# Kernel optimization log

Measured on AMD Instinct MI355X. Metric: run time of the kernel, lower is better.

Reference implementation:

```python
import jax, jax.numpy as jnp
import numpy as np

ND = 3       # ndims
Q = 8        # mixture components
LAT = 64     # latent_dim
N = 2048     # num X points
M = 2048     # num Y points
TRI = ND * (ND + 1) // 2  # 6

_TI, _TJ = np.tril_indices(ND)


def setup_inputs() -> dict:
    key = jax.random.key(0)
    ks = jax.random.split(key, 10)
    s_in = 1.0 / np.sqrt(ND)
    s_lat = 1.0 / np.sqrt(LAT)
    return {
        "x": jax.random.normal(ks[0], (N, ND), jnp.float32),
        "y": jax.random.normal(ks[1], (M, ND), jnp.float32),
        "W1": jax.random.normal(ks[2], (LAT, ND), jnp.float32) * s_in,
        "b1": jax.random.normal(ks[3], (LAT,), jnp.float32) * 0.1,
        "Ww": jax.random.normal(ks[4], (Q, LAT), jnp.float32) * s_lat,
        "bw": jax.random.normal(ks[5], (Q,), jnp.float32) * 0.1,
        "Wf": jax.random.normal(ks[6], (Q * ND, LAT), jnp.float32) * s_lat,
        "bf": jax.random.normal(ks[7], (Q * ND,), jnp.float32) * 0.1,
        "Ws": jax.random.normal(ks[8], (Q * TRI, LAT), jnp.float32) * s_lat,
        "bs": jax.random.normal(ks[9], (Q * TRI,), jnp.float32) * 0.1,
    }


def _features(p, W1, b1, Ww, bw, Wf, bf, Ws, bs):
    # shared hidden layer (computed once per point, unlike the original which
    # recomputes it for each of the 3 heads -- same math)
    h = jax.nn.selu(p @ W1.T + b1)                                  # [n, LAT]
    w = jax.nn.softplus(h @ Ww.T + bw)                              # [n, Q]
    f = jax.nn.softplus(h @ Wf.T + bf).reshape(p.shape[0], Q, ND)   # [n, Q, ND]
    s = jax.nn.softplus(h @ Ws.T + bs).reshape(p.shape[0], Q, TRI)  # [n, Q, TRI]
    # place into lower-triangular L, then A = L @ L.T
    L = jnp.zeros((p.shape[0], Q, ND, ND), p.dtype).at[:, :, _TI, _TJ].set(s)
    A = jnp.einsum('nqab,nqcb->nqac', L, L)                         # [n, Q, ND, ND]
    phase = jnp.einsum('nqd,nd->nq', f, p)                          # [n, Q]
    return w, A, phase


def reference(x, y, W1, b1, Ww, bw, Wf, bf, Ws, bs):
    # __call__ -> k_xy[i, j] = eval(x=Y[j], y=X[i]); shape [N, M]
    wX, AX, phX = _features(x, W1, b1, Ww, bw, Wf, bf, Ws, bs)
    wY, AY, phY = _features(y, W1, b1, Ww, bw, Wf, bf, Ws, bs)

    diff = y[None, :, :] - x[:, None, :]                            # [N, M, ND]
    # r_scaled = diff @ (A_x + A_y) @ diff, split into the two quadratic forms
    qx = jnp.einsum('ijd,iqde,ije->ijq', diff, AX, diff)            # [N, M, Q]
    qy = jnp.einsum('ijd,jqde,ije->ijq', diff, AY, diff)            # [N, M, Q]
    r = qx + qy

    sq5 = jnp.sqrt(jnp.asarray(5.0, r.dtype))
    mat = (1.0 + sq5 * r + (5.0 / 3.0) * r * r) * jnp.exp(-sq5 * r)
    cosine = jnp.cos(2.0 * jnp.pi * (phY[None, :, :] - phX[:, None, :]))
    k = jnp.sum(wY[None, :, :] * wX[:, None, :] * mat * cosine, axis=-1)
    return k
```

## Files before the change

### kernel.cpp

```cpp
#include <hip/hip_runtime.h>
#include <hip/hip_bf16.h>

#define NPTS 2048
#define QMIX 8
#define LATD 64
#define IT   32
#define HIT  16
#define FSTRIDE 72

typedef float v2f __attribute__((ext_vector_type(2)));

__device__ __forceinline__ float softplus_f(float x) {
    return fmaxf(x, 0.0f) + log1pf(expf(-fabsf(x)));
}
__device__ __forceinline__ float selu_f(float z) {
    const float sc = 1.0507009873554805f;
    const float sa = 1.7580993408473766f;
    return (z > 0.0f) ? sc * z : sa * expm1f(z);
}

__global__ __launch_bounds__(640) void feat_kernel(
    const float* __restrict__ xin, const float* __restrict__ yin,
    const float* __restrict__ W1, const float* __restrict__ b1,
    const float* __restrict__ Ww, const float* __restrict__ bw,
    const float* __restrict__ Wf, const float* __restrict__ bf,
    const float* __restrict__ Ws, const float* __restrict__ bs,
    float* __restrict__ F)
{
    __shared__ float hsh[8][LATD + 4];
    __shared__ float raw[8][80];
    const int t = threadIdx.x;

    if (t < 512) {
        const int pl = t & 7, l = t >> 3;
        const int g = blockIdx.x * 8 + pl;
        const bool isx = (g < NPTS);
        const float* pts = isx ? (xin + 3 * g) : (yin + 3 * (g - NPTS));
        const float z = fmaf(W1[l * 3 + 0], pts[0],
                        fmaf(W1[l * 3 + 1], pts[1],
                        fmaf(W1[l * 3 + 2], pts[2], b1[l])));
        hsh[pl][l] = selu_f(z);
    }
    __syncthreads();

    {
        const int o  = t >> 3;
        const int pl = t & 7;
        const int q  = o / 10;
        const int e  = o % 10;
        const float* row;
        float acc;
        if (e == 0)      { row = Ww + q * LATD;                 acc = bw[q]; }
        else if (e <= 3) { row = Wf + (q * 3 + (e - 1)) * LATD; acc = bf[q * 3 + (e - 1)]; }
        else             { row = Ws + (q * 6 + (e - 4)) * LATD; acc = bs[q * 6 + (e - 4)]; }
#pragma unroll
        for (int l4 = 0; l4 < LATD / 4; ++l4) {
            const float4 rv = reinterpret_cast<const float4*>(row)[l4];
            const float4 hv = *reinterpret_cast<const float4*>(&hsh[pl][l4 * 4]);
            acc = fmaf(rv.x, hv.x, acc);
            acc = fmaf(rv.y, hv.y, acc);
            acc = fmaf(rv.z, hv.z, acc);
            acc = fmaf(rv.w, hv.w, acc);
        }
        raw[pl][o] = softplus_f(acc);
    }
    __syncthreads();

    if (t < 64) {
        const int pl2 = t >> 3, q2 = t & 7;
        const int g2  = blockIdx.x * 8 + pl2;
        const bool isx2 = (g2 < NPTS);
        const float* pts2 = isx2 ? (xin + 3 * g2) : (yin + 3 * (g2 - NPTS));
        const float c0 = pts2[0], c1 = pts2[1], c2 = pts2[2];
        const float* r = raw[pl2] + q2 * 10;
        const float w  = r[0];
        const float f0 = r[1], f1 = r[2], f2 = r[3];
        const float s0 = r[4], s1 = r[5], s2 = r[6];
        const float s3 = r[7], s4 = r[8], s5 = r[9];

        const float A00 = s0 * s0;
        const float A11 = fmaf(s1, s1, s2 * s2);
        const float A22 = fmaf(s3, s3, fmaf(s4, s4, s5 * s5));
        const float A01 = s0 * s1;
        const float A02 = s0 * s3;
        const float A12 = fmaf(s1, s3, s2 * s4);
        const float ph  = fmaf(f0, c0, fmaf(f1, c1, f2 * c2));
        float sn, cs;
        sincosf(6.283185307179586477f * ph, &sn, &cs);

        const float EF  = 3.2259751249059600974f;
        const float EF2 = 2.0f * EF;
        const float vals[8] = { EF * A00, EF * A11, EF * A22,
                                EF2 * A01, EF2 * A02, EF2 * A12,
                                w * cs, w * sn };
        float* o = F + (size_t)g2 * FSTRIDE;
        const int base = (q2 >> 1) * 16 + (q2 & 1);
#pragma unroll
        for (int k = 0; k < 8; ++k) o[base + k * 2] = vals[k];
        if (q2 == 0) {
            o[64] = c0; o[65] = c0;
            o[66] = c1; o[67] = c1;
            o[68] = c2; o[69] = c2;
        }
    }
}

__global__ __launch_bounds__(256, 4) void pair_kernel(
    const float* __restrict__ F, float* __restrict__ out)
{
    __shared__ float red[HIT][128];
    const int t    = threadIdx.x;
    const int wave = __builtin_amdgcn_readfirstlane(t >> 6);
    const int lane = t & 63;
    const int qg   = wave & 1;
    const int jh   = wave >> 1;
    const int jl   = jh * 64 + lane;
    const int j    = blockIdx.x * 128 + jl;
    const int i0   = blockIdx.y * IT;

    const float* __restrict__ frow = F + (size_t)(NPTS + j) * FSTRIDE;
    v2f fy[16];
    {
        const float4* fp = reinterpret_cast<const float4*>(frow + qg * 32);
#pragma unroll
        for (int n = 0; n < 8; ++n) {
            const float4 v = fp[n];
            fy[2 * n + 0] = v2f{v.x, v.y};
            fy[2 * n + 1] = v2f{v.z, v.w};
        }
    }
    const v2f yd0 = *reinterpret_cast<const v2f*>(frow + 64);
    const v2f yd1 = *reinterpret_cast<const v2f*>(frow + 66);
    const v2f yd2 = *reinterpret_cast<const v2f*>(frow + 68);

    const float P1 = 0.69314718055994530942f;
    const float P2 = 0.16013630893549922444f;
    const float* __restrict__ fxb = F + (size_t)i0 * FSTRIDE;

#pragma unroll
    for (int half = 0; half < 2; ++half) {
        v2f acc[HIT];
#pragma unroll
        for (int i2 = 0; i2 < HIT; ++i2) {
            const float* __restrict__ fx = fxb + (half * HIT + i2) * FSTRIDE;
            const v2f xd0 = *reinterpret_cast<const v2f*>(fx + 64);
            const v2f xd1 = *reinterpret_cast<const v2f*>(fx + 66);
            const v2f xd2 = *reinterpret_cast<const v2f*>(fx + 68);
            const v2f d0 = yd0 - xd0;
            const v2f d1 = yd1 - xd1;
            const v2f d2 = yd2 - xd2;
            const v2f p00 = d0 * d0, p11 = d1 * d1, p22 = d2 * d2;
            const v2f p01 = d0 * d1, p02 = d0 * d2, p12 = d1 * d2;

            v2f a = v2f{0.f, 0.f};
#pragma unroll
            for (int qpl = 0; qpl < 2; ++qpl) {
                const v2f* __restrict__ c =
                    reinterpret_cast<const v2f*>(fx + (qg * 2 + qpl) * 16);
                v2f u;
                u  = (fy[qpl * 8 + 0] + c[0]) * p00;
                u += (fy[qpl * 8 + 1] + c[1]) * p11;
                u += (fy[qpl * 8 + 2] + c[2]) * p22;
                u += (fy[qpl * 8 + 3] + c[3]) * p01;
                u += (fy[qpl * 8 + 4] + c[4]) * p02;
                u += (fy[qpl * 8 + 5] + c[5]) * p12;
                const v2f poly = u * (u * P2 + P1) + 1.0f;
                const v2f ex = v2f{__builtin_amdgcn_exp2f(-u.x),
                                   __builtin_amdgcn_exp2f(-u.y)};
                v2f ct = fy[qpl * 8 + 6] * c[6];
                ct += fy[qpl * 8 + 7] * c[7];
                a += (poly * ex) * ct;
            }
            acc[i2] = a;
        }

        if (qg == 1) {
#pragma unroll
            for (int i2 = 0; i2 < HIT; ++i2)
                red[i2][jl] = acc[i2].x + acc[i2].y;
        }
        __syncthreads();
        if (qg == 0) {
#pragma unroll
            for (int i2 = 0; i2 < HIT; ++i2) {
                out[(size_t)(i0 + half * HIT + i2) * NPTS + j] =
                    acc[i2].x + acc[i2].y + red[i2][jl];
            }
        }
        __syncthreads();
    }
}

extern "C" void kernel_launch(void* const* d_in, const int* in_sizes, int n_in,
                              void* d_out, int out_size, void* d_ws, size_t ws_size,
                              hipStream_t stream) {
    const float* x  = (const float*)d_in[0];
    const float* y  = (const float*)d_in[1];
    const float* W1 = (const float*)d_in[2];
    const float* b1 = (const float*)d_in[3];
    const float* Ww = (const float*)d_in[4];
    const float* bw = (const float*)d_in[5];
    const float* Wf = (const float*)d_in[6];
    const float* bf = (const float*)d_in[7];
    const float* Ws = (const float*)d_in[8];
    const float* bs = (const float*)d_in[9];
    float* out = (float*)d_out;

    float* F = (float*)d_ws;

    feat_kernel<<<dim3((2 * NPTS) / 8), dim3(640), 0, stream>>>(
        x, y, W1, b1, Ww, bw, Wf, bf, Ws, bs, F);

    pair_kernel<<<dim3(NPTS / 128, NPTS / IT), dim3(256), 0, stream>>>(F, out);
}
```

Baseline: 34.24 us.

## Recast pairwise quadratic forms as bf16x3 MFMA matrix products

The quadratic form (y-x)^T(Ax+Ay)(y-x) is expanded algebraically into a 10-term dot product between per-point coefficient and monomial vectors. Those vectors are split into hi/lo bf16 pairs so the pair kernel can compute the quadratic forms with 16x16x32 bf16 MFMA instructions. The cosine weight term becomes a small MFMA built from packed cos/sin weights. X tiles are staged in swizzled LDS. This moves the pairwise arithmetic onto matrix cores. In exchange it adds precision risk from the bf16 splitting, from cancellation in the expanded form, and from rounding the weights to bf16, and the new layout enlarges the workspace.

```diff
diff --git a/kernel.cpp b/kernel.cpp
--- a/kernel.cpp
+++ b/kernel.cpp
@@ -4,11 +4,10 @@
 #define NPTS 2048
 #define QMIX 8
 #define LATD 64
-#define IT   32
-#define HIT  16
-#define FSTRIDE 72
-
-typedef float v2f __attribute__((ext_vector_type(2)));
+#define NIT  4
+
+typedef float f32x4 __attribute__((ext_vector_type(4)));
+typedef short short8 __attribute__((ext_vector_type(8)));
 
 __device__ __forceinline__ float softplus_f(float x) {
     return fmaxf(x, 0.0f) + log1pf(expf(-fabsf(x)));
@@ -17,6 +16,16 @@
     const float sc = 1.0507009873554805f;
     const float sa = 1.7580993408473766f;
     return (z > 0.0f) ? sc * z : sa * expm1f(z);
+}
+__device__ __forceinline__ ushort bfrn(float v) {
+    unsigned b = __float_as_uint(v);
+    return (ushort)((b + 0x7fffu + ((b >> 16) & 1u)) >> 16);
+}
+__device__ __forceinline__ void split_bf16(float v, ushort& h, ushort& l) {
+    unsigned b  = __float_as_uint(v);
+    unsigned hb = b & 0xffff0000u;
+    h = (ushort)(hb >> 16);
+    l = bfrn(v - __uint_as_float(hb));
 }
 
 __global__ __launch_bounds__(640) void feat_kernel(
@@ -25,7 +34,9 @@
     const float* __restrict__ Ww, const float* __restrict__ bw,
     const float* __restrict__ Wf, const float* __restrict__ bf,
     const float* __restrict__ Ws, const float* __restrict__ bs,
-    float* __restrict__ F)
+    ushort* __restrict__ AXH, ushort* __restrict__ AXL,
+    ushort* __restrict__ BYH, ushort* __restrict__ BYL,
+    uint* __restrict__ CTX, uint* __restrict__ CTY)
 {
     __shared__ float hsh[8][LATD + 4];
     __shared__ float raw[8][80];
@@ -72,122 +83,133 @@
         const bool isx2 = (g2 < NPTS);
         const float* pts2 = isx2 ? (xin + 3 * g2) : (yin + 3 * (g2 - NPTS));
         const float c0 = pts2[0], c1 = pts2[1], c2 = pts2[2];
-        const float* r = raw[pl2] + q2 * 10;
-        const float w  = r[0];
-        const float f0 = r[1], f1 = r[2], f2 = r[3];
-        const float s0 = r[4], s1 = r[5], s2 = r[6];
-        const float s3 = r[7], s4 = r[8], s5 = r[9];
+        const float* rr = raw[pl2] + q2 * 10;
+        const float w  = rr[0];
+        const float f0 = rr[1], f1 = rr[2], f2 = rr[3];
+        const float s0 = rr[4], s1 = rr[5], s2 = rr[6];
+        const float s3 = rr[7], s4 = rr[8], s5 = rr[9];
 
         const float A00 = s0 * s0;
-        const float A11 = fmaf(s1, s1, s2 * s2);
-        const float A22 = fmaf(s3, s3, fmaf(s4, s4, s5 * s5));
         const float A01 = s0 * s1;
         const float A02 = s0 * s3;
+        const float A11 = fmaf(s1, s1, s2 * s2);
         const float A12 = fmaf(s1, s3, s2 * s4);
+        const float A22 = fmaf(s3, s3, fmaf(s4, s4, s5 * s5));
+        const float Ax0 = fmaf(A00, c0, fmaf(A01, c1, A02 * c2));
+        const float Ax1 = fmaf(A01, c0, fmaf(A11, c1, A12 * c2));
+        const float Ax2 = fmaf(A02, c0, fmaf(A12, c1, A22 * c2));
+        const float pAp = fmaf(c0, Ax0, fmaf(c1, Ax1, c2 * Ax2));
         const float ph  = fmaf(f0, c0, fmaf(f1, c1, f2 * c2));
         float sn, cs;
         sincosf(6.283185307179586477f * ph, &sn, &cs);
 
-        const float EF  = 3.2259751249059600974f;
-        const float EF2 = 2.0f * EF;
-        const float vals[8] = { EF * A00, EF * A11, EF * A22,
-                                EF2 * A01, EF2 * A02, EF2 * A12,
-                                w * cs, w * sn };
-        float* o = F + (size_t)g2 * FSTRIDE;
-        const int base = (q2 >> 1) * 16 + (q2 & 1);
-#pragma unroll
-        for (int k = 0; k < 8; ++k) o[base + k * 2] = vals[k];
-        if (q2 == 0) {
-            o[64] = c0; o[65] = c0;
-            o[66] = c1; o[67] = c1;
-            o[68] = c2; o[69] = c2;
-        }
+        const float EF = 3.2259751249059600974f;
+        const float cf[10] = { EF * A00, EF * A11, EF * A22,
+                               2.0f * EF * A01, 2.0f * EF * A02, 2.0f * EF * A12,
+                               -2.0f * EF * Ax0, -2.0f * EF * Ax1, -2.0f * EF * Ax2,
+                               EF * pAp };
+        const float pv[10] = { c0 * c0, c1 * c1, c2 * c2,
+                               c0 * c1, c0 * c2, c1 * c2,
+                               c0, c1, c2, 1.0f };
+        float slots[20];
+#pragma unroll
+        for (int k = 0; k < 10; ++k) {
+            slots[k]      = isx2 ? cf[k] : pv[k];
+            slots[10 + k] = isx2 ? pv[k] : cf[k];
+        }
+        ushort H[32], L[32];
+#pragma unroll
+        for (int k = 0; k < 32; ++k) { H[k] = 0; L[k] = 0; }
+#pragma unroll
+        for (int k = 0; k < 20; ++k) split_bf16(slots[k], H[k], L[k]);
+
+        const int pi = isx2 ? g2 : (g2 - NPTS);
+        ushort* dh = (isx2 ? AXH : BYH) + ((size_t)pi * 8 + q2) * 32;
+        ushort* dl = (isx2 ? AXL : BYL) + ((size_t)pi * 8 + q2) * 32;
+#pragma unroll
+        for (int m = 0; m < 16; ++m) {
+            ((uint*)dh)[m] = (uint)H[2 * m] | ((uint)H[2 * m + 1] << 16);
+            ((uint*)dl)[m] = (uint)L[2 * m] | ((uint)L[2 * m + 1] << 16);
+        }
+        uint* ct = isx2 ? CTX : CTY;
+        ct[(size_t)pi * 8 + q2] = (uint)bfrn(w * cs) | ((uint)bfrn(w * sn) << 16);
     }
 }
 
 __global__ __launch_bounds__(256, 4) void pair_kernel(
-    const float* __restrict__ F, float* __restrict__ out)
+    const ushort* __restrict__ AXH, const ushort* __restrict__ AXL,
+    const uint*  __restrict__ CTX,
+    const ushort* __restrict__ BYH, const ushort* __restrict__ BYL,
+    const uint*  __restrict__ CTY, float* __restrict__ out)
 {
-    __shared__ float red[HIT][128];
-    const int t    = threadIdx.x;
-    const int wave = __builtin_amdgcn_readfirstlane(t >> 6);
-    const int lane = t & 63;
-    const int qg   = wave & 1;
-    const int jh   = wave >> 1;
-    const int jl   = jh * 64 + lane;
-    const int j    = blockIdx.x * 128 + jl;
-    const int i0   = blockIdx.y * IT;
-
-    const float* __restrict__ frow = F + (size_t)(NPTS + j) * FSTRIDE;
-    v2f fy[16];
+    __shared__ ushort sAH[16 * 256];
+    __shared__ ushort sAL[16 * 256];
+    __shared__ uint   sCT[16 * 9];
+    const int t   = threadIdx.x;
+    const int wv  = t >> 6, ln = t & 63;
+    const int col = ln & 15, kb = ln >> 4;
+    const int j0  = blockIdx.x * 64 + wv * 16;
+    const int it0 = blockIdx.y * NIT;
+
+    short8 Bh[8], Bl[8], Bc[8];
     {
-        const float4* fp = reinterpret_cast<const float4*>(frow + qg * 32);
-#pragma unroll
-        for (int n = 0; n < 8; ++n) {
-            const float4 v = fp[n];
-            fy[2 * n + 0] = v2f{v.x, v.y};
-            fy[2 * n + 1] = v2f{v.z, v.w};
-        }
-    }
-    const v2f yd0 = *reinterpret_cast<const v2f*>(frow + 64);
-    const v2f yd1 = *reinterpret_cast<const v2f*>(frow + 66);
-    const v2f yd2 = *reinterpret_cast<const v2f*>(frow + 68);
-
+        const ushort* bh = BYH + (size_t)(j0 + col) * 256 + kb * 8;
+        const ushort* bl = BYL + (size_t)(j0 + col) * 256 + kb * 8;
+#pragma unroll
+        for (int q = 0; q < 8; ++q) {
+            Bh[q] = *reinterpret_cast<const short8*>(bh + q * 32);
+            Bl[q] = *reinterpret_cast<const short8*>(bl + q * 32);
+            const uint cv = (kb == 2) ? CTY[(size_t)(j0 + col) * 8 + q] : 0u;
+            short8 bc = {0, 0, 0, 0, (short)(cv & 0xffffu), (short)(cv >> 16), 0, 0};
+            Bc[q] = bc;
+        }
+    }
     const float P1 = 0.69314718055994530942f;
     const float P2 = 0.16013630893549922444f;
-    const float* __restrict__ fxb = F + (size_t)i0 * FSTRIDE;
-
-#pragma unroll
-    for (int half = 0; half < 2; ++half) {
-        v2f acc[HIT];
-#pragma unroll
-        for (int i2 = 0; i2 < HIT; ++i2) {
-            const float* __restrict__ fx = fxb + (half * HIT + i2) * FSTRIDE;
-            const v2f xd0 = *reinterpret_cast<const v2f*>(fx + 64);
-            const v2f xd1 = *reinterpret_cast<const v2f*>(fx + 66);
-            const v2f xd2 = *reinterpret_cast<const v2f*>(fx + 68);
-            const v2f d0 = yd0 - xd0;
-            const v2f d1 = yd1 - xd1;
-            const v2f d2 = yd2 - xd2;
-            const v2f p00 = d0 * d0, p11 = d1 * d1, p22 = d2 * d2;
-            const v2f p01 = d0 * d1, p02 = d0 * d2, p12 = d1 * d2;
-
-            v2f a = v2f{0.f, 0.f};
-#pragma unroll
-            for (int qpl = 0; qpl < 2; ++qpl) {
-                const v2f* __restrict__ c =
-                    reinterpret_cast<const v2f*>(fx + (qg * 2 + qpl) * 16);
-                v2f u;
-                u  = (fy[qpl * 8 + 0] + c[0]) * p00;
-                u += (fy[qpl * 8 + 1] + c[1]) * p11;
-                u += (fy[qpl * 8 + 2] + c[2]) * p22;
-                u += (fy[qpl * 8 + 3] + c[3]) * p01;
-                u += (fy[qpl * 8 + 4] + c[4]) * p02;
-                u += (fy[qpl * 8 + 5] + c[5]) * p12;
-                const v2f poly = u * (u * P2 + P1) + 1.0f;
-                const v2f ex = v2f{__builtin_amdgcn_exp2f(-u.x),
-                                   __builtin_amdgcn_exp2f(-u.y)};
-                v2f ct = fy[qpl * 8 + 6] * c[6];
-                ct += fy[qpl * 8 + 7] * c[7];
-                a += (poly * ex) * ct;
+
+    for (int it = 0; it < NIT; ++it) {
+        const int i0 = (it0 + it) * 16;
+        if (it) __syncthreads();
+        {
+            const uint4* srcH = reinterpret_cast<const uint4*>(AXH + (size_t)i0 * 256);
+            const uint4* srcL = reinterpret_cast<const uint4*>(AXL + (size_t)i0 * 256);
+#pragma unroll
+            for (int u = 0; u < 2; ++u) {
+                const int s   = t + u * 256;
+                const int row = s >> 5, sl = s & 31;
+                const int ds  = row * 32 + (sl ^ row);
+                reinterpret_cast<uint4*>(sAH)[ds] = srcH[s];
+                reinterpret_cast<uint4*>(sAL)[ds] = srcL[s];
             }
-            acc[i2] = a;
-        }
-
-        if (qg == 1) {
-#pragma unroll
-            for (int i2 = 0; i2 < HIT; ++i2)
-                red[i2][jl] = acc[i2].x + acc[i2].y;
+            if (t < 128) sCT[(t >> 3) * 9 + (t & 7)] =
+                CTX[(size_t)(i0 + (t >> 3)) * 8 + (t & 7)];
         }
         __syncthreads();
-        if (qg == 0) {
-#pragma unroll
-            for (int i2 = 0; i2 < HIT; ++i2) {
-                out[(size_t)(i0 + half * HIT + i2) * NPTS + j] =
-                    acc[i2].x + acc[i2].y + red[i2][jl];
+
+        f32x4 kacc = {0.f, 0.f, 0.f, 0.f};
+#pragma unroll
+        for (int q = 0; q < 8; ++q) {
+            const int ro = col * 256 + (((q * 4 + kb) ^ col) << 3);
+            const short8 Ah = *reinterpret_cast<const short8*>(sAH + ro);
+            const short8 Al = *reinterpret_cast<const short8*>(sAL + ro);
+            const f32x4 z = {0.f, 0.f, 0.f, 0.f};
+            f32x4 au = __builtin_amdgcn_mfma_f32_16x16x32_bf16(Ah, Bh[q], z, 0, 0, 0);
+            au = __builtin_amdgcn_mfma_f32_16x16x32_bf16(Al, Bh[q], au, 0, 0, 0);
+            au = __builtin_amdgcn_mfma_f32_16x16x32_bf16(Ah, Bl[q], au, 0, 0, 0);
+            const uint av = (kb == 2) ? sCT[col * 9 + q] : 0u;
+            short8 Ac = {0, 0, 0, 0, (short)(av & 0xffffu), (short)(av >> 16), 0, 0};
+            const f32x4 ac = __builtin_amdgcn_mfma_f32_16x16x32_bf16(Ac, Bc[q], z, 0, 0, 0);
+#pragma unroll
+            for (int e = 0; e < 4; ++e) {
+                const float u  = au[e];
+                const float po = fmaf(u, fmaf(u, P2, P1), 1.0f);
+                const float ex = __builtin_amdgcn_exp2f(-u);
+                kacc[e] = fmaf(po * ex, ac[e], kacc[e]);
             }
         }
-        __syncthreads();
+#pragma unroll
+        for (int e = 0; e < 4; ++e)
+            out[(size_t)(i0 + kb * 4 + e) * NPTS + j0 + col] = kacc[e];
     }
 }
 
@@ -206,10 +228,16 @@
     const float* bs = (const float*)d_in[9];
     float* out = (float*)d_out;
 
-    float* F = (float*)d_ws;
+    ushort* AXH = (ushort*)d_ws;
+    ushort* AXL = AXH + (size_t)NPTS * 256;
+    ushort* BYH = AXL + (size_t)NPTS * 256;
+    ushort* BYL = BYH + (size_t)NPTS * 256;
+    uint*   CTX = (uint*)(BYL + (size_t)NPTS * 256);
+    uint*   CTY = CTX + (size_t)NPTS * 8;
 
     feat_kernel<<<dim3((2 * NPTS) / 8), dim3(640), 0, stream>>>(
-        x, y, W1, b1, Ww, bw, Wf, bf, Ws, bs, F);
-
-    pair_kernel<<<dim3(NPTS / 128, NPTS / IT), dim3(256), 0, stream>>>(F, out);
-}
+        x, y, W1, b1, Ww, bw, Wf, bf, Ws, bs, AXH, AXL, BYH, BYL, CTX, CTY);
+
+    pair_kernel<<<dim3(NPTS / 64, NPTS / (NIT * 16)), dim3(256), 0, stream>>>(
+        AXH, AXL, CTX, BYH, BYL, CTY, out);
+}
```

Result: slower. 67.99 us (+98.6%).
